# Kernel optimization log

Measured on AMD Instinct MI355X. Metric: run time of the kernel, lower is better.

Reference implementation:

```python
import jax, jax.numpy as jnp
import numpy as np

B, T, E, H, V = 64, 32, 300, 1024, 10000


def setup_inputs() -> dict:
    key = jax.random.key(0)
    ks = jax.random.split(key, 12)
    s = lambda fan: 1.0 / np.sqrt(fan)
    return {
        "questions": jax.random.randint(ks[0], (B, T), 0, V, dtype=jnp.int64) if jax.config.jax_enable_x64 else jax.random.randint(ks[0], (B, T), 0, V, dtype=jnp.int32),
        "question_lengths": jax.random.randint(ks[1], (B,), 1, T + 1, dtype=jnp.int32),
        "embed_table": jax.random.normal(ks[2], (V, E), jnp.float32) * 0.02,
        "W_ih1": jax.random.normal(ks[3], (4 * H, E), jnp.float32) * s(H),
        "W_hh1": jax.random.normal(ks[4], (4 * H, H), jnp.float32) * s(H),
        "b_ih1": jax.random.normal(ks[5], (4 * H,), jnp.float32) * s(H),
        "b_hh1": jax.random.normal(ks[6], (4 * H,), jnp.float32) * s(H),
        "W_ih2": jax.random.normal(ks[7], (4 * H, H), jnp.float32) * s(H),
        "W_hh2": jax.random.normal(ks[8], (4 * H, H), jnp.float32) * s(H),
        "b_ih2": jax.random.normal(ks[9], (4 * H,), jnp.float32) * s(H),
        "b_hh2": jax.random.normal(ks[10], (4 * H,), jnp.float32) * s(H),
    }


def _lstm_cell(x_t, h, c, W_ih, W_hh, b_ih, b_hh):
    # PyTorch LSTMCell: gate order i, f, g, o
    gates = x_t @ W_ih.T + b_ih + h @ W_hh.T + b_hh  # [B, 4H]
    i, f, g, o = jnp.split(gates, 4, axis=-1)
    c_new = jax.nn.sigmoid(f) * c + jax.nn.sigmoid(i) * jnp.tanh(g)
    h_new = jax.nn.sigmoid(o) * jnp.tanh(c_new)
    return h_new, c_new


def reference(questions, question_lengths, embed_table,
              W_ih1, W_hh1, b_ih1, b_hh1, W_ih2, W_hh2, b_ih2, b_hh2):
    x = embed_table[questions]                      # [B, T, E]
    b, t, _ = x.shape
    h = W_hh1.shape[1]

    def step(carry, inp):
        h1, c1, h2, c2 = carry
        x_t, m = inp                                # x_t [B,E], m [B,1] bool
        h1n, c1n = _lstm_cell(x_t, h1, c1, W_ih1, W_hh1, b_ih1, b_hh1)
        h2n, c2n = _lstm_cell(h1n, h2, c2, W_ih2, W_hh2, b_ih2, b_hh2)
        # samples past their length keep their final state frozen
        h1 = jnp.where(m, h1n, h1); c1 = jnp.where(m, c1n, c1)
        h2 = jnp.where(m, h2n, h2); c2 = jnp.where(m, c2n, c2)
        return (h1, c1, h2, c2), None

    mask = jnp.arange(t)[None, :] < question_lengths[:, None]      # [B,T]
    xs = (jnp.swapaxes(x, 0, 1), jnp.swapaxes(mask, 0, 1)[..., None])
    init = tuple(jnp.zeros((b, h), x.dtype) for _ in range(4))
    (h1, c1, h2, c2), _ = jax.lax.scan(step, init, xs)

    # tile final top-layer hidden to [B, H, 28, 28]
    E_q = jnp.broadcast_to(h2[:, None, None, :], (b, 28, 28, h))
    E_q = jnp.transpose(E_q, (0, 3, 2, 1))
    return (E_q, h1[:, None, :], h2[:, None, :], c1[:, None, :], c2[:, None, :])
```

## Files before the change

kernel.cpp:

```cpp
#include <hip/hip_runtime.h>
#include <hip/hip_bf16.h>
#include <cstdint>

#define B_  64
#define T_  32
#define E_  300
#define EP  320
#define H_  1024
#define G4  4096
#define BH  65536
#define NBLK 192

typedef __attribute__((ext_vector_type(8))) short bf16x8;
typedef __attribute__((ext_vector_type(4))) float f32x4;
typedef unsigned short ushort_t;

__device__ __forceinline__ bf16x8 load_b8(const ushort_t* p) {
    union { uint4 u; bf16x8 v; } c;
    c.u = *reinterpret_cast<const uint4*>(p);
    return c.v;
}

__device__ __forceinline__ ushort_t f2bf(float x) {
    union { float f; uint32_t u; } c; c.f = x;
    uint32_t r = c.u + 0x7fffu + ((c.u >> 16) & 1u);
    return (ushort_t)(r >> 16);
}

__device__ __forceinline__ float sigm(float x) { return 1.0f / (1.0f + __expf(-x)); }

__device__ __forceinline__ void astore64(uint64_t* p, uint64_t v) {
    __hip_atomic_store(p, v, __ATOMIC_RELAXED, __HIP_MEMORY_SCOPE_AGENT);
}
__device__ __forceinline__ uint64_t packf2(float a, float b) {
    union { float f[2]; uint64_t u; } c; c.f[0] = a; c.f[1] = b; return c.u;
}

__device__ __forceinline__ void setflag(int* flags, int role, int js, int val) {
    __hip_atomic_store(&flags[(role * 64 + js) * 16], val,
                       __ATOMIC_RELAXED, __HIP_MEMORY_SCOPE_AGENT);
}
__device__ __forceinline__ void waitwave(const int* flags, int role, int target, int lane) {
    const int* p = &flags[(role * 64 + lane) * 16];
    int guard = 0;
    for (;;) {
        int v = __hip_atomic_load(p, __ATOMIC_RELAXED, __HIP_MEMORY_SCOPE_AGENT);
        if (__all(v >= target)) return;
        if (++guard > (1 << 22)) return;
        __builtin_amdgcn_s_sleep(1);
    }
}

__global__ void prep_inputs(const int* __restrict__ q, const float* __restrict__ table,
                            ushort_t* __restrict__ Xp,
                            const float* __restrict__ Wsrc, ushort_t* __restrict__ Wdst,
                            ushort_t* __restrict__ h1s0, ushort_t* __restrict__ h2s0) {
    int blk = blockIdx.x;
    if (blk < 1280) {
        int i = blk * 256 + threadIdx.x;
        const int n = B_ * T_ * EP;
        for (; i < n; i += 1280 * 256) {
            int r = i / EP, c = i - r * EP;
            Xp[i] = (c < E_) ? f2bf(table[q[r] * E_ + c]) : (ushort_t)0;
        }
    } else if (blk < 3328) {
        int i = (blk - 1280) * 256 + threadIdx.x;
        const int n = G4 * EP;
        for (; i < n; i += 2048 * 256) {
            int r = i / EP, c = i - r * EP;
            Wdst[i] = (c < E_) ? f2bf(Wsrc[r * E_ + c]) : (ushort_t)0;
        }
    } else {
        int i = (blk - 3328) * 256 + threadIdx.x;
        uint4 z = make_uint4(0, 0, 0, 0);
        if (i < 8192) reinterpret_cast<uint4*>(h1s0)[i] = z;
        else          reinterpret_cast<uint4*>(h2s0)[i - 8192] = z;
    }
}

__launch_bounds__(256)
__global__ void xgemm(const ushort_t* __restrict__ Xp, const ushort_t* __restrict__ Wp,
                      const float* __restrict__ b_ih1, const float* __restrict__ b_hh1,
                      float* __restrict__ xg) {
    int mblk = blockIdx.x, nblk = blockIdx.y;
    int wave = threadIdx.x >> 6, lane = threadIdx.x & 63;
    int lm = lane & 15, lq = lane >> 4;
    int m0 = mblk * 64 + wave * 16;
    f32x4 acc[4];
    #pragma unroll
    for (int g = 0; g < 4; ++g) {
        int n = nblk * 64 + g * 16 + lm;
        float bv = b_ih1[n] + b_hh1[n];
        acc[g] = (f32x4){bv, bv, bv, bv};
    }
    for (int k0 = 0; k0 < EP; k0 += 32) {
        bf16x8 a = load_b8(Xp + (m0 + lm) * EP + k0 + lq * 8);
        #pragma unroll
        for (int g = 0; g < 4; ++g) {
            bf16x8 b = load_b8(Wp + (nblk * 64 + g * 16 + lm) * EP + k0 + lq * 8);
            acc[g] = __builtin_amdgcn_mfma_f32_16x16x32_bf16(a, b, acc[g], 0, 0, 0);
        }
    }
    #pragma unroll
    for (int g = 0; g < 4; ++g)
        #pragma unroll
        for (int r = 0; r < 4; ++r) {
            int m = m0 + lq * 4 + r;
            int b = m >> 5, t = m & 31;
            int n = nblk * 64 + g * 16 + lm;
            int gate = n >> 10, j = n & 1023;
            xg[(((size_t)t * B_ + b) * H_ + j) * 4 + gate] = acc[g][r];
        }
}


__device__ __forceinline__ void gemm_half(const ushort_t* __restrict__ hslot,
                                          const ushort_t* __restrict__ wsf,
                                          int lm, int lq, int m0, int kh, f32x4 acc[4]) {
    const uint4* hr = reinterpret_cast<const uint4*>(hslot);
    const int rbase = (m0 + lm) * 2 + (lq & 1);
    const int cbo = lq >> 1;
    const int cb0 = kh * 32;
    uint4 buf[16];
    #pragma unroll
    for (int grp = 0; grp < 2; ++grp)
        #pragma unroll
        for (int i = 0; i < 8; ++i)
            buf[grp * 8 + i] = hr[(cb0 + grp * 16 + i * 2 + cbo) * 128 + rbase];
    #pragma unroll
    for (int grp = 0; grp < 2; ++grp)
        #pragma unroll
        for (int i = 0; i < 8; ++i) {
            int k0 = kh * 512 + grp * 256 + i * 32;
            union { uint4 u; bf16x8 v; } a; a.u = buf[grp * 8 + i];
            #pragma unroll
            for (int g = 0; g < 4; ++g) {
                int row = g * 16 + lm;
                bf16x8 bb = load_b8(wsf + row * 1024 + ((k0 + lq * 8) ^ ((lm & 7) << 3)));
                acc[g] = __builtin_amdgcn_mfma_f32_16x16x32_bf16(a.v, bb, acc[g], 0, 0, 0);
            }
        }
}

__device__ __forceinline__ void lstm_elem(const f32x4 acc[4], int r,
                                          float* c, float* h, ushort_t* hb) {
    float iv = sigm(acc[0][r]);
    float fv = sigm(acc[1][r]);
    float gv = tanhf(acc[2][r]);
    float ov = sigm(acc[3][r]);
    float cn = fv * c[r] + iv * gv;
    float hv = ov * tanhf(cn);
    c[r] = cn; h[r] = hv; hb[r] = f2bf(hv);
}

__device__ __forceinline__ void store_h_tile(ushort_t* slot, int js, const ushort_t* hst) {
    int tid = threadIdx.x;
    uint64_t v = reinterpret_cast<const uint64_t*>(hst)[tid];
    astore64(reinterpret_cast<uint64_t*>(slot) + js * 256 + tid, v);
}

__global__ __launch_bounds__(512) void lstm_persist(
    const float* __restrict__ Whh1, const float* __restrict__ Wih2,
    const float* __restrict__ Whh2,
    const float* __restrict__ b_ih2, const float* __restrict__ b_hh2,
    const float* __restrict__ xg, const int* __restrict__ qlen,
    ushort_t* __restrict__ h1hist,
    ushort_t* __restrict__ h2hist,
    float* __restrict__ Qhist,
    float* __restrict__ h1f, float* __restrict__ c1f,
    float* __restrict__ h2f, float* __restrict__ c2f,
    int* __restrict__ flags)
{
    __shared__ ushort_t ws[64 * 1024];
    __shared__ __align__(16) ushort_t hstage[64][16];
    __shared__ f32x4 pacc[256][4];

    const int blk  = blockIdx.x;
    const int role = blk >> 6;
    const int js   = blk & 63;
    const int w    = threadIdx.x >> 6, lane = threadIdx.x & 63;
    const int mi   = w & 3, kh = w >> 2;
    const int lm = lane & 15, lq = lane >> 4;
    const int m0 = mi * 16;
    const int pidx = mi * 64 + lane;

    const float* Wsrc = (role == 0) ? Whh1 : (role == 1) ? Wih2 : Whh2;
    uint2* wsp = reinterpret_cast<uint2*>(ws);
    for (int idx = threadIdx.x; idx < 64 * 256; idx += 512) {
        int r = idx >> 8, c4 = idx & 255;
        int grow = (r >> 4) * H_ + js * 16 + (r & 15);
        float4 v = reinterpret_cast<const float4*>(Wsrc + (size_t)grow * H_)[c4];
        uint2 pk;
        pk.x = (uint32_t)f2bf(v.x) | ((uint32_t)f2bf(v.y) << 16);
        pk.y = (uint32_t)f2bf(v.z) | ((uint32_t)f2bf(v.w) << 16);
        wsp[r * 256 + (c4 ^ ((r & 7) << 1))] = pk;
    }
    __syncthreads();

    int q[4];
    #pragma unroll
    for (int r = 0; r < 4; ++r) q[r] = qlen[m0 + lq * 4 + r];

    float    c_reg[4]  = {0.f, 0.f, 0.f, 0.f};
    float    h_reg[4]  = {0.f, 0.f, 0.f, 0.f};
    ushort_t hb_reg[4] = {0, 0, 0, 0};

    if (role == 0) {
        for (int t = 0; t < T_; ++t) {
            f32x4 acc[4];
            #pragma unroll
            for (int g = 0; g < 4; ++g) acc[g] = (f32x4){0.f, 0.f, 0.f, 0.f};
            if (kh == 0) {
                uint4 xq[4];
                #pragma unroll
                for (int r = 0; r < 4; ++r)
                    xq[r] = reinterpret_cast<const uint4*>(xg)
                            [((size_t)t * B_ + (m0 + lq * 4 + r)) * H_ + js * 16 + lm];
                #pragma unroll
                for (int r = 0; r < 4; ++r) {
                    union { uint32_t u; float f; } x0, x1, x2, x3;
                    x0.u = xq[r].x; x1.u = xq[r].y; x2.u = xq[r].z; x3.u = xq[r].w;
                    acc[0][r] = x0.f; acc[1][r] = x1.f;
                    acc[2][r] = x2.f; acc[3][r] = x3.f;
                }
            }
            if (t > 0) {
                if (w == 0) waitwave(flags, 0, t, lane);
                __syncthreads();
            }
            gemm_half(h1hist + (size_t)t * BH, ws, lm, lq, m0, kh, acc);
            if (kh == 1) {
                #pragma unroll
                for (int g = 0; g < 4; ++g) pacc[pidx][g] = acc[g];
            }
            __syncthreads();
            if (kh == 0) {
                #pragma unroll
                for (int g = 0; g < 4; ++g) acc[g] += pacc[pidx][g];
                #pragma unroll
                for (int r = 0; r < 4; ++r) {
                    if (t < q[r]) lstm_elem(acc, r, c_reg, h_reg, hb_reg);
                    hstage[m0 + lq * 4 + r][lm] = hb_reg[r];
                }
            }
            __syncthreads();
            if (threadIdx.x < 256)
                store_h_tile(h1hist + (size_t)(t + 1) * BH, js, &hstage[0][0]);
            __syncthreads();
            if (threadIdx.x == 0) setflag(flags, 0, js, t + 1);
        }
        if (kh == 0) {
            #pragma unroll
            for (int r = 0; r < 4; ++r) {
                int b = m0 + lq * 4 + r, j = js * 16 + lm;
                h1f[b * H_ + j] = h_reg[r]; c1f[b * H_ + j] = c_reg[r];
            }
        }
    } else if (role == 1) {
        float bi[4];
        #pragma unroll
        for (int g = 0; g < 4; ++g) {
            int n = g * H_ + js * 16 + lm;
            bi[g] = b_ih2[n] + b_hh2[n];
        }
        for (int t = 0; t < T_; ++t) {
            if (w == 0) waitwave(flags, 0, t + 1, lane);
            __syncthreads();
            f32x4 acc[4];
            #pragma unroll
            for (int g = 0; g < 4; ++g)
                acc[g] = (kh == 0) ? (f32x4){bi[g], bi[g], bi[g], bi[g]}
                                   : (f32x4){0.f, 0.f, 0.f, 0.f};
            gemm_half(h1hist + (size_t)(t + 1) * BH, ws, lm, lq, m0, kh, acc);
            if (kh == 1) {
                #pragma unroll
                for (int g = 0; g < 4; ++g) pacc[pidx][g] = acc[g];
            }
            __syncthreads();
            if (kh == 0) {
                #pragma unroll
                for (int g = 0; g < 4; ++g) acc[g] += pacc[pidx][g];
                uint64_t* Qw64 = (uint64_t*)(Qhist + (size_t)t * (4 * BH));
                #pragma unroll
                for (int r = 0; r < 4; ++r) {
                    int b = m0 + lq * 4 + r, j = js * 16 + lm;
                    size_t base = ((size_t)b * H_ + j) * 2;
                    astore64(Qw64 + base,     packf2(acc[0][r], acc[1][r]));
                    astore64(Qw64 + base + 1, packf2(acc[2][r], acc[3][r]));
                }
            }
            __syncthreads();
            if (threadIdx.x == 0) setflag(flags, 1, js, t + 1);
        }
    } else {
        for (int t = 0; t < T_; ++t) {
            if (w == 0)               waitwave(flags, 1, t + 1, lane);
            else if (w == 1 && t > 0) waitwave(flags, 2, t,     lane);
            __syncthreads();
            uint4 qp[4];
            if (kh == 0) {
                const uint4* Qr = (const uint4*)(Qhist + (size_t)t * (4 * BH));
                #pragma unroll
                for (int r = 0; r < 4; ++r)
                    qp[r] = Qr[(size_t)(m0 + lq * 4 + r) * H_ + js * 16 + lm];
            }
            f32x4 acc[4];
            #pragma unroll
            for (int g = 0; g < 4; ++g) acc[g] = (f32x4){0.f, 0.f, 0.f, 0.f};
            gemm_half(h2hist + (size_t)t * BH, ws, lm, lq, m0, kh, acc);
            if (kh == 1) {
                #pragma unroll
                for (int g = 0; g < 4; ++g) pacc[pidx][g] = acc[g];
            }
            __syncthreads();
            if (kh == 0) {
                #pragma unroll
                for (int g = 0; g < 4; ++g) acc[g] += pacc[pidx][g];
                #pragma unroll
                for (int r = 0; r < 4; ++r) {
                    union { uint32_t u; float f; } x0, x1, x2, x3;
                    x0.u = qp[r].x; x1.u = qp[r].y; x2.u = qp[r].z; x3.u = qp[r].w;
                    acc[0][r] += x0.f; acc[1][r] += x1.f;
                    acc[2][r] += x2.f; acc[3][r] += x3.f;
                }
                #pragma unroll
                for (int r = 0; r < 4; ++r) {
                    if (t < q[r]) lstm_elem(acc, r, c_reg, h_reg, hb_reg);
                    hstage[m0 + lq * 4 + r][lm] = hb_reg[r];
                }
            }
            __syncthreads();
            if (threadIdx.x < 256)
                store_h_tile(h2hist + (size_t)(t + 1) * BH, js, &hstage[0][0]);
            __syncthreads();
            if (t < T_ - 1 && threadIdx.x == 0) setflag(flags, 2, js, t + 1);
        }
        if (kh == 0) {
            #pragma unroll
            for (int r = 0; r < 4; ++r) {
                int b = m0 + lq * 4 + r, j = js * 16 + lm;
                h2f[b * H_ + j] = h_reg[r]; c2f[b * H_ + j] = c_reg[r];
            }
        }
    }
}

__global__ void write_out(const float* __restrict__ h1f, const float* __restrict__ h2f,
                          const float* __restrict__ c1f, const float* __restrict__ c2f,
                          float* __restrict__ out) {
    const long long EQ = (long long)B_ * H_ * 784;
    const long long n4 = (EQ + 4LL * B_ * H_) / 4;
    long long i4 = (long long)blockIdx.x * blockDim.x + threadIdx.x;
    long long stride = (long long)gridDim.x * blockDim.x;
    for (; i4 < n4; i4 += stride) {
        long long f = i4 * 4;
        float4 v;
        if (f < EQ) {
            long long bh = f / 784;
            float val = h2f[bh];
            v = make_float4(val, val, val, val);
        } else {
            long long r = f - EQ;
            int which = (int)(r >> 16);
            int j = (int)(r & 65535);
            const float* src = (which == 0) ? h1f : (which == 1) ? h2f : (which == 2) ? c1f : c2f;
            v = *reinterpret_cast<const float4*>(src + j);
        }
        reinterpret_cast<float4*>(out)[i4] = v;
    }
}

extern "C" void kernel_launch(void* const* d_in, const int* in_sizes, int n_in,
                              void* d_out, int out_size, void* d_ws, size_t ws_size,
                              hipStream_t stream) {
    const int*   questions = (const int*)d_in[0];
    const int*   qlen      = (const int*)d_in[1];
    const float* embed     = (const float*)d_in[2];
    const float* W_ih1     = (const float*)d_in[3];
    const float* W_hh1     = (const float*)d_in[4];
    const float* b_ih1     = (const float*)d_in[5];
    const float* b_hh1     = (const float*)d_in[6];
    const float* W_ih2     = (const float*)d_in[7];
    const float* W_hh2     = (const float*)d_in[8];
    const float* b_ih2     = (const float*)d_in[9];
    const float* b_hh2     = (const float*)d_in[10];
    float* out = (float*)d_out;

    char* w = (char*)d_ws;
    float*    xg     = (float*)(w + 0);
    ushort_t* Wih1p  = (ushort_t*)(w + 33554432);
    ushort_t* Xp     = (ushort_t*)(w + 36175872);
    int*      flags  = (int*)(w + 36175872);
    ushort_t* h1hist = (ushort_t*)(w + 37486592);
    ushort_t* h2hist = (ushort_t*)(w + 41811968);
    float*    Qhist  = (float*)(w + 46137344);
    float*    h1f    = (float*)(w + 79691776);
    float*    c1f    = (float*)(w + 79953920);
    float*    h2f    = (float*)(w + 80216064);
    float*    c2f    = (float*)(w + 80478208);

    prep_inputs<<<3392, 256, 0, stream>>>(questions, embed, Xp, W_ih1, Wih1p,
                                          h1hist, h2hist);
    xgemm<<<dim3(32, 64), 256, 0, stream>>>(Xp, Wih1p, b_ih1, b_hh1, xg);

    hipMemsetAsync(w + 36175872, 0, 12288, stream);

    lstm_persist<<<NBLK, 512, 0, stream>>>(W_hh1, W_ih2, W_hh2, b_ih2, b_hh2,
                                           xg, qlen,
                                           h1hist, h2hist, Qhist,
                                           h1f, c1f, h2f, c2f, flags);

    write_out<<<4096, 256, 0, stream>>>(h1f, h2f, c1f, c2f, out);
}
```

Measured before the change: 529.3 us.

## Keep recurrent weight slices in registers and split K across four waves

The persistent LSTM kernel no longer stages its 64x1024 bf16 weight slice in shared memory. Each wave now holds its K-quarter of the weights as MFMA B-fragments in registers and covers two 16-row M tiles, so it no longer reads weights from LDS on every step. Partial sums from the four K-quarters are reduced through a smaller shared buffer, and the flag zeroing moves from a separate memset into the prep kernel at a new workspace offset. The cost is heavy register pressure (32 bf16x8 fragments plus accumulators per lane), which may cause spills, and a three-way LDS reduction on every step.

New measurement: 727.0 us. 1.37x slower.

```diff
diff --git a/kernel.cpp b/kernel.cpp
--- a/kernel.cpp
+++ b/kernel.cpp
@@ -54,7 +54,8 @@
 __global__ void prep_inputs(const int* __restrict__ q, const float* __restrict__ table,
                             ushort_t* __restrict__ Xp,
                             const float* __restrict__ Wsrc, ushort_t* __restrict__ Wdst,
-                            ushort_t* __restrict__ h1s0, ushort_t* __restrict__ h2s0) {
+                            ushort_t* __restrict__ h1s0, ushort_t* __restrict__ h2s0,
+                            int* __restrict__ flags) {
     int blk = blockIdx.x;
     if (blk < 1280) {
         int i = blk * 256 + threadIdx.x;
@@ -70,11 +71,14 @@
             int r = i / EP, c = i - r * EP;
             Wdst[i] = (c < E_) ? f2bf(Wsrc[r * E_ + c]) : (ushort_t)0;
         }
-    } else {
+    } else if (blk < 3392) {
         int i = (blk - 3328) * 256 + threadIdx.x;
         uint4 z = make_uint4(0, 0, 0, 0);
         if (i < 8192) reinterpret_cast<uint4*>(h1s0)[i] = z;
         else          reinterpret_cast<uint4*>(h2s0)[i - 8192] = z;
+    } else {
+        int i = (blk - 3392) * 256 + threadIdx.x;
+        reinterpret_cast<uint4*>(flags)[i] = make_uint4(0, 0, 0, 0);
     }
 }
 
@@ -114,43 +118,30 @@
 }
 
 
-__device__ __forceinline__ void gemm_half(const ushort_t* __restrict__ hslot,
-                                          const ushort_t* __restrict__ wsf,
-                                          int lm, int lq, int m0, int kh, f32x4 acc[4]) {
-    const uint4* hr = reinterpret_cast<const uint4*>(hslot);
-    const int rbase = (m0 + lm) * 2 + (lq & 1);
-    const int cbo = lq >> 1;
-    const int cb0 = kh * 32;
-    uint4 buf[16];
+__device__ __forceinline__ void gemm_q(const uint4* __restrict__ hr,
+                                       const bf16x8 (&wfr)[32],
+                                       int rbase, int cbase, f32x4 acc[2][4]) {
     #pragma unroll
-    for (int grp = 0; grp < 2; ++grp)
-        #pragma unroll
-        for (int i = 0; i < 8; ++i)
-            buf[grp * 8 + i] = hr[(cb0 + grp * 16 + i * 2 + cbo) * 128 + rbase];
-    #pragma unroll
-    for (int grp = 0; grp < 2; ++grp)
+    for (int half = 0; half < 2; ++half) {
+        uint4 af[8];
         #pragma unroll
         for (int i = 0; i < 8; ++i) {
-            int k0 = kh * 512 + grp * 256 + i * 32;
-            union { uint4 u; bf16x8 v; } a; a.u = buf[grp * 8 + i];
+            int kc = half * 4 + (i >> 1), mi = i & 1;
+            af[i] = hr[cbase + kc * 256 + rbase + mi * 32];
+        }
+        #pragma unroll
+        for (int k4 = 0; k4 < 4; ++k4) {
+            int kc = half * 4 + k4;
             #pragma unroll
-            for (int g = 0; g < 4; ++g) {
-                int row = g * 16 + lm;
-                bf16x8 bb = load_b8(wsf + row * 1024 + ((k0 + lq * 8) ^ ((lm & 7) << 3)));
-                acc[g] = __builtin_amdgcn_mfma_f32_16x16x32_bf16(a.v, bb, acc[g], 0, 0, 0);
-            }
-        }
-}
-
-__device__ __forceinline__ void lstm_elem(const f32x4 acc[4], int r,
-                                          float* c, float* h, ushort_t* hb) {
-    float iv = sigm(acc[0][r]);
-    float fv = sigm(acc[1][r]);
-    float gv = tanhf(acc[2][r]);
-    float ov = sigm(acc[3][r]);
-    float cn = fv * c[r] + iv * gv;
-    float hv = ov * tanhf(cn);
-    c[r] = cn; h[r] = hv; hb[r] = f2bf(hv);
+            for (int mi = 0; mi < 2; ++mi) {
+                union { uint4 u; bf16x8 v; } a; a.u = af[k4 * 2 + mi];
+                #pragma unroll
+                for (int nt = 0; nt < 4; ++nt)
+                    acc[mi][nt] = __builtin_amdgcn_mfma_f32_16x16x32_bf16(
+                        a.v, wfr[nt * 8 + kc], acc[mi][nt], 0, 0, 0);
+            }
+        }
+    }
 }
 
 __device__ __forceinline__ void store_h_tile(ushort_t* slot, int js, const ushort_t* hst) {
@@ -159,7 +150,7 @@
     astore64(reinterpret_cast<uint64_t*>(slot) + js * 256 + tid, v);
 }
 
-__global__ __launch_bounds__(512) void lstm_persist(
+__global__ __launch_bounds__(512, 2) void lstm_persist(
     const float* __restrict__ Whh1, const float* __restrict__ Wih2,
     const float* __restrict__ Whh2,
     const float* __restrict__ b_ih2, const float* __restrict__ b_hh2,
@@ -171,77 +162,103 @@
     float* __restrict__ h2f, float* __restrict__ c2f,
     int* __restrict__ flags)
 {
-    __shared__ ushort_t ws[64 * 1024];
+    __shared__ f32x4 pacc[8][6][64];
     __shared__ __align__(16) ushort_t hstage[64][16];
-    __shared__ f32x4 pacc[256][4];
 
     const int blk  = blockIdx.x;
     const int role = blk >> 6;
     const int js   = blk & 63;
     const int w    = threadIdx.x >> 6, lane = threadIdx.x & 63;
-    const int mi   = w & 3, kh = w >> 2;
+    const int kq   = w & 3, mh = w >> 2;
     const int lm = lane & 15, lq = lane >> 4;
-    const int m0 = mi * 16;
-    const int pidx = mi * 64 + lane;
 
     const float* Wsrc = (role == 0) ? Whh1 : (role == 1) ? Wih2 : Whh2;
-    uint2* wsp = reinterpret_cast<uint2*>(ws);
-    for (int idx = threadIdx.x; idx < 64 * 256; idx += 512) {
-        int r = idx >> 8, c4 = idx & 255;
-        int grow = (r >> 4) * H_ + js * 16 + (r & 15);
-        float4 v = reinterpret_cast<const float4*>(Wsrc + (size_t)grow * H_)[c4];
-        uint2 pk;
-        pk.x = (uint32_t)f2bf(v.x) | ((uint32_t)f2bf(v.y) << 16);
-        pk.y = (uint32_t)f2bf(v.z) | ((uint32_t)f2bf(v.w) << 16);
-        wsp[r * 256 + (c4 ^ ((r & 7) << 1))] = pk;
-    }
-    __syncthreads();
-
-    int q[4];
+    bf16x8 wfr[32];
     #pragma unroll
-    for (int r = 0; r < 4; ++r) q[r] = qlen[m0 + lq * 4 + r];
-
-    float    c_reg[4]  = {0.f, 0.f, 0.f, 0.f};
-    float    h_reg[4]  = {0.f, 0.f, 0.f, 0.f};
-    ushort_t hb_reg[4] = {0, 0, 0, 0};
+    for (int nt = 0; nt < 4; ++nt)
+        #pragma unroll
+        for (int kc = 0; kc < 8; ++kc) {
+            const float* p = Wsrc + (size_t)(nt * H_ + js * 16 + lm) * H_
+                           + kq * 256 + kc * 32 + lq * 8;
+            float4 v0 = *reinterpret_cast<const float4*>(p);
+            float4 v1 = *reinterpret_cast<const float4*>(p + 4);
+            union { uint32_t u[4]; bf16x8 v; } c;
+            c.u[0] = (uint32_t)f2bf(v0.x) | ((uint32_t)f2bf(v0.y) << 16);
+            c.u[1] = (uint32_t)f2bf(v0.z) | ((uint32_t)f2bf(v0.w) << 16);
+            c.u[2] = (uint32_t)f2bf(v1.x) | ((uint32_t)f2bf(v1.y) << 16);
+            c.u[3] = (uint32_t)f2bf(v1.z) | ((uint32_t)f2bf(v1.w) << 16);
+            wfr[nt * 8 + kc] = c.v;
+        }
+
+    const int rbase = (mh * 32 + lm) * 2 + (lq & 1);
+    const int cbase = (kq * 16 + (lq >> 1)) * 128;
+
+    int q[2][4];
+    #pragma unroll
+    for (int mi = 0; mi < 2; ++mi)
+        #pragma unroll
+        for (int r = 0; r < 4; ++r)
+            q[mi][r] = qlen[mh * 32 + mi * 16 + lq * 4 + r];
+
+    float    c_reg[2][4] = {};
+    float    h_reg[2][4] = {};
+    ushort_t hb_reg[2][4] = {};
 
     if (role == 0) {
         for (int t = 0; t < T_; ++t) {
-            f32x4 acc[4];
-            #pragma unroll
-            for (int g = 0; g < 4; ++g) acc[g] = (f32x4){0.f, 0.f, 0.f, 0.f};
-            if (kh == 0) {
-                uint4 xq[4];
-                #pragma unroll
-                for (int r = 0; r < 4; ++r)
-                    xq[r] = reinterpret_cast<const uint4*>(xg)
-                            [((size_t)t * B_ + (m0 + lq * 4 + r)) * H_ + js * 16 + lm];
-                #pragma unroll
-                for (int r = 0; r < 4; ++r) {
-                    union { uint32_t u; float f; } x0, x1, x2, x3;
-                    x0.u = xq[r].x; x1.u = xq[r].y; x2.u = xq[r].z; x3.u = xq[r].w;
-                    acc[0][r] = x0.f; acc[1][r] = x1.f;
-                    acc[2][r] = x2.f; acc[3][r] = x3.f;
-                }
-            }
             if (t > 0) {
                 if (w == 0) waitwave(flags, 0, t, lane);
                 __syncthreads();
             }
-            gemm_half(h1hist + (size_t)t * BH, ws, lm, lq, m0, kh, acc);
-            if (kh == 1) {
-                #pragma unroll
-                for (int g = 0; g < 4; ++g) pacc[pidx][g] = acc[g];
-            }
-            __syncthreads();
-            if (kh == 0) {
-                #pragma unroll
-                for (int g = 0; g < 4; ++g) acc[g] += pacc[pidx][g];
-                #pragma unroll
-                for (int r = 0; r < 4; ++r) {
-                    if (t < q[r]) lstm_elem(acc, r, c_reg, h_reg, hb_reg);
-                    hstage[m0 + lq * 4 + r][lm] = hb_reg[r];
-                }
+            f32x4 acc[2][4] = {};
+            gemm_q(reinterpret_cast<const uint4*>(h1hist + (size_t)t * BH),
+                   wfr, rbase, cbase, acc);
+            uint4 xq[8];
+            if (kq == 0) {
+                #pragma unroll
+                for (int mi = 0; mi < 2; ++mi)
+                    #pragma unroll
+                    for (int r = 0; r < 4; ++r)
+                        xq[mi * 4 + r] = reinterpret_cast<const uint4*>(xg)
+                            [((size_t)t * B_ + (mh * 32 + mi * 16 + lq * 4 + r)) * H_ + js * 16 + lm];
+            } else {
+                #pragma unroll
+                for (int mi = 0; mi < 2; ++mi)
+                    #pragma unroll
+                    for (int nt = 0; nt < 4; ++nt)
+                        pacc[mi * 4 + nt][mh * 3 + (kq - 1)][lane] = acc[mi][nt];
+            }
+            __syncthreads();
+            if (kq == 0) {
+                #pragma unroll
+                for (int s = 0; s < 3; ++s)
+                    #pragma unroll
+                    for (int mi = 0; mi < 2; ++mi)
+                        #pragma unroll
+                        for (int nt = 0; nt < 4; ++nt)
+                            acc[mi][nt] += pacc[mi * 4 + nt][mh * 3 + s][lane];
+                #pragma unroll
+                for (int mi = 0; mi < 2; ++mi)
+                    #pragma unroll
+                    for (int r = 0; r < 4; ++r) {
+                        union { uint32_t u; float f; } x0, x1, x2, x3;
+                        x0.u = xq[mi * 4 + r].x; x1.u = xq[mi * 4 + r].y;
+                        x2.u = xq[mi * 4 + r].z; x3.u = xq[mi * 4 + r].w;
+                        float a0 = acc[0][0][0];
+                        (void)a0;
+                        float g0 = acc[mi][0][r] + x0.f;
+                        float g1 = acc[mi][1][r] + x1.f;
+                        float g2 = acc[mi][2][r] + x2.f;
+                        float g3 = acc[mi][3][r] + x3.f;
+                        if (t < q[mi][r]) {
+                            float iv = sigm(g0), fv = sigm(g1);
+                            float gv = tanhf(g2), ov = sigm(g3);
+                            float cn = fv * c_reg[mi][r] + iv * gv;
+                            float hv = ov * tanhf(cn);
+                            c_reg[mi][r] = cn; h_reg[mi][r] = hv; hb_reg[mi][r] = f2bf(hv);
+                        }
+                        hstage[mh * 32 + mi * 16 + lq * 4 + r][lm] = hb_reg[mi][r];
+                    }
             }
             __syncthreads();
             if (threadIdx.x < 256)
@@ -249,12 +266,14 @@
             __syncthreads();
             if (threadIdx.x == 0) setflag(flags, 0, js, t + 1);
         }
-        if (kh == 0) {
+        if (kq == 0) {
             #pragma unroll
-            for (int r = 0; r < 4; ++r) {
-                int b = m0 + lq * 4 + r, j = js * 16 + lm;
-                h1f[b * H_ + j] = h_reg[r]; c1f[b * H_ + j] = c_reg[r];
-            }
+            for (int mi = 0; mi < 2; ++mi)
+                #pragma unroll
+                for (int r = 0; r < 4; ++r) {
+                    int b = mh * 32 + mi * 16 + lq * 4 + r, j = js * 16 + lm;
+                    h1f[b * H_ + j] = h_reg[mi][r]; c1f[b * H_ + j] = c_reg[mi][r];
+                }
         }
     } else if (role == 1) {
         float bi[4];
@@ -266,28 +285,37 @@
         for (int t = 0; t < T_; ++t) {
             if (w == 0) waitwave(flags, 0, t + 1, lane);
             __syncthreads();
-            f32x4 acc[4];
-            #pragma unroll
-            for (int g = 0; g < 4; ++g)
-                acc[g] = (kh == 0) ? (f32x4){bi[g], bi[g], bi[g], bi[g]}
-                                   : (f32x4){0.f, 0.f, 0.f, 0.f};
-            gemm_half(h1hist + (size_t)(t + 1) * BH, ws, lm, lq, m0, kh, acc);
-            if (kh == 1) {
-                #pragma unroll
-                for (int g = 0; g < 4; ++g) pacc[pidx][g] = acc[g];
-            }
-            __syncthreads();
-            if (kh == 0) {
-                #pragma unroll
-                for (int g = 0; g < 4; ++g) acc[g] += pacc[pidx][g];
+            f32x4 acc[2][4] = {};
+            gemm_q(reinterpret_cast<const uint4*>(h1hist + (size_t)(t + 1) * BH),
+                   wfr, rbase, cbase, acc);
+            if (kq != 0) {
+                #pragma unroll
+                for (int mi = 0; mi < 2; ++mi)
+                    #pragma unroll
+                    for (int nt = 0; nt < 4; ++nt)
+                        pacc[mi * 4 + nt][mh * 3 + (kq - 1)][lane] = acc[mi][nt];
+            }
+            __syncthreads();
+            if (kq == 0) {
+                #pragma unroll
+                for (int s = 0; s < 3; ++s)
+                    #pragma unroll
+                    for (int mi = 0; mi < 2; ++mi)
+                        #pragma unroll
+                        for (int nt = 0; nt < 4; ++nt)
+                            acc[mi][nt] += pacc[mi * 4 + nt][mh * 3 + s][lane];
                 uint64_t* Qw64 = (uint64_t*)(Qhist + (size_t)t * (4 * BH));
                 #pragma unroll
-                for (int r = 0; r < 4; ++r) {
-                    int b = m0 + lq * 4 + r, j = js * 16 + lm;
-                    size_t base = ((size_t)b * H_ + j) * 2;
-                    astore64(Qw64 + base,     packf2(acc[0][r], acc[1][r]));
-                    astore64(Qw64 + base + 1, packf2(acc[2][r], acc[3][r]));
-                }
+                for (int mi = 0; mi < 2; ++mi)
+                    #pragma unroll
+                    for (int r = 0; r < 4; ++r) {
+                        int b = mh * 32 + mi * 16 + lq * 4 + r, j = js * 16 + lm;
+                        size_t base = ((size_t)b * H_ + j) * 2;
+                        astore64(Qw64 + base,
+                                 packf2(acc[mi][0][r] + bi[0], acc[mi][1][r] + bi[1]));
+                        astore64(Qw64 + base + 1,
+                                 packf2(acc[mi][2][r] + bi[2], acc[mi][3][r] + bi[3]));
+                    }
             }
             __syncthreads();
             if (threadIdx.x == 0) setflag(flags, 1, js, t + 1);
@@ -297,37 +325,53 @@
             if (w == 0)               waitwave(flags, 1, t + 1, lane);
             else if (w == 1 && t > 0) waitwave(flags, 2, t,     lane);
             __syncthreads();
-            uint4 qp[4];
-            if (kh == 0) {
+            f32x4 acc[2][4] = {};
+            gemm_q(reinterpret_cast<const uint4*>(h2hist + (size_t)t * BH),
+                   wfr, rbase, cbase, acc);
+            uint4 qp[8];
+            if (kq == 0) {
                 const uint4* Qr = (const uint4*)(Qhist + (size_t)t * (4 * BH));
                 #pragma unroll
-                for (int r = 0; r < 4; ++r)
-                    qp[r] = Qr[(size_t)(m0 + lq * 4 + r) * H_ + js * 16 + lm];
-            }
-            f32x4 acc[4];
-            #pragma unroll
-            for (int g = 0; g < 4; ++g) acc[g] = (f32x4){0.f, 0.f, 0.f, 0.f};
-            gemm_half(h2hist + (size_t)t * BH, ws, lm, lq, m0, kh, acc);
-            if (kh == 1) {
-                #pragma unroll
-                for (int g = 0; g < 4; ++g) pacc[pidx][g] = acc[g];
-            }
-            __syncthreads();
-            if (kh == 0) {
-                #pragma unroll
-                for (int g = 0; g < 4; ++g) acc[g] += pacc[pidx][g];
-                #pragma unroll
-                for (int r = 0; r < 4; ++r) {
-                    union { uint32_t u; float f; } x0, x1, x2, x3;
-                    x0.u = qp[r].x; x1.u = qp[r].y; x2.u = qp[r].z; x3.u = qp[r].w;
-                    acc[0][r] += x0.f; acc[1][r] += x1.f;
-                    acc[2][r] += x2.f; acc[3][r] += x3.f;
-                }
-                #pragma unroll
-                for (int r = 0; r < 4; ++r) {
-                    if (t < q[r]) lstm_elem(acc, r, c_reg, h_reg, hb_reg);
-                    hstage[m0 + lq * 4 + r][lm] = hb_reg[r];
-                }
+                for (int mi = 0; mi < 2; ++mi)
+                    #pragma unroll
+                    for (int r = 0; r < 4; ++r)
+                        qp[mi * 4 + r] = Qr[(size_t)(mh * 32 + mi * 16 + lq * 4 + r) * H_ + js * 16 + lm];
+            } else {
+                #pragma unroll
+                for (int mi = 0; mi < 2; ++mi)
+                    #pragma unroll
+                    for (int nt = 0; nt < 4; ++nt)
+                        pacc[mi * 4 + nt][mh * 3 + (kq - 1)][lane] = acc[mi][nt];
+            }
+            __syncthreads();
+            if (kq == 0) {
+                #pragma unroll
+                for (int s = 0; s < 3; ++s)
+                    #pragma unroll
+                    for (int mi = 0; mi < 2; ++mi)
+                        #pragma unroll
+                        for (int nt = 0; nt < 4; ++nt)
+                            acc[mi][nt] += pacc[mi * 4 + nt][mh * 3 + s][lane];
+                #pragma unroll
+                for (int mi = 0; mi < 2; ++mi)
+                    #pragma unroll
+                    for (int r = 0; r < 4; ++r) {
+                        union { uint32_t u; float f; } x0, x1, x2, x3;
+                        x0.u = qp[mi * 4 + r].x; x1.u = qp[mi * 4 + r].y;
+                        x2.u = qp[mi * 4 + r].z; x3.u = qp[mi * 4 + r].w;
+                        float g0 = acc[mi][0][r] + x0.f;
+                        float g1 = acc[mi][1][r] + x1.f;
+                        float g2 = acc[mi][2][r] + x2.f;
+                        float g3 = acc[mi][3][r] + x3.f;
+                        if (t < q[mi][r]) {
+                            float iv = sigm(g0), fv = sigm(g1);
+                            float gv = tanhf(g2), ov = sigm(g3);
+                            float cn = fv * c_reg[mi][r] + iv * gv;
+                            float hv = ov * tanhf(cn);
+                            c_reg[mi][r] = cn; h_reg[mi][r] = hv; hb_reg[mi][r] = f2bf(hv);
+                        }
+                        hstage[mh * 32 + mi * 16 + lq * 4 + r][lm] = hb_reg[mi][r];
+                    }
             }
             __syncthreads();
             if (threadIdx.x < 256)
@@ -335,12 +379,14 @@
             __syncthreads();
             if (t < T_ - 1 && threadIdx.x == 0) setflag(flags, 2, js, t + 1);
         }
-        if (kh == 0) {
+        if (kq == 0) {
             #pragma unroll
-            for (int r = 0; r < 4; ++r) {
-                int b = m0 + lq * 4 + r, j = js * 16 + lm;
-                h2f[b * H_ + j] = h_reg[r]; c2f[b * H_ + j] = c_reg[r];
-            }
+            for (int mi = 0; mi < 2; ++mi)
+                #pragma unroll
+                for (int r = 0; r < 4; ++r) {
+                    int b = mh * 32 + mi * 16 + lq * 4 + r, j = js * 16 + lm;
+                    h2f[b * H_ + j] = h_reg[mi][r]; c2f[b * H_ + j] = c_reg[mi][r];
+                }
         }
     }
 }
@@ -390,7 +436,6 @@
     float*    xg     = (float*)(w + 0);
     ushort_t* Wih1p  = (ushort_t*)(w + 33554432);
     ushort_t* Xp     = (ushort_t*)(w + 36175872);
-    int*      flags  = (int*)(w + 36175872);
     ushort_t* h1hist = (ushort_t*)(w + 37486592);
     ushort_t* h2hist = (ushort_t*)(w + 41811968);
     float*    Qhist  = (float*)(w + 46137344);
@@ -398,12 +443,11 @@
     float*    c1f    = (float*)(w + 79953920);
     float*    h2f    = (float*)(w + 80216064);
     float*    c2f    = (float*)(w + 80478208);
-
-    prep_inputs<<<3392, 256, 0, stream>>>(questions, embed, Xp, W_ih1, Wih1p,
-                                          h1hist, h2hist);
+    int*      flags  = (int*)(w + 80740352);
+
+    prep_inputs<<<3395, 256, 0, stream>>>(questions, embed, Xp, W_ih1, Wih1p,
+                                          h1hist, h2hist, flags);
     xgemm<<<dim3(32, 64), 256, 0, stream>>>(Xp, Wih1p, b_ih1, b_hh1, xg);
-
-    hipMemsetAsync(w + 36175872, 0, 12288, stream);
 
     lstm_persist<<<NBLK, 512, 0, stream>>>(W_hh1, W_ih2, W_hh2, b_ih2, b_hh2,
                                            xg, qlen,
```

## Fuse output writes into persistent LSTM kernel and fold flag reset into prep

Applied to the files above, without the earlier changes.

Drops the separate write_out kernel. Each sample's final h/c states and its broadcast 28x28 E_q tile are now written from inside the persistent LSTM kernel, at the timestep where that sample's length ends. The flag memset moves into extra blocks of prep_inputs, removing two launches. The cost is that the roughly 205 MB E_q broadcast now runs inside the latency-bound recurrence loop on only 64 blocks, which could stretch the critical path.

Result: slower. 607.8 us (+14.8%).

```diff
diff --git a/kernel.cpp b/kernel.cpp
--- a/kernel.cpp
+++ b/kernel.cpp
@@ -11,6 +11,12 @@
 #define BH  65536
 #define NBLK 192
 
+#define EQOFF 0LL
+#define H1OFF 51380224LL
+#define H2OFF 51445760LL
+#define C1OFF 51511296LL
+#define C2OFF 51576832LL
+
 typedef __attribute__((ext_vector_type(8))) short bf16x8;
 typedef __attribute__((ext_vector_type(4))) float f32x4;
 typedef unsigned short ushort_t;
@@ -54,7 +60,8 @@
 __global__ void prep_inputs(const int* __restrict__ q, const float* __restrict__ table,
                             ushort_t* __restrict__ Xp,
                             const float* __restrict__ Wsrc, ushort_t* __restrict__ Wdst,
-                            ushort_t* __restrict__ h1s0, ushort_t* __restrict__ h2s0) {
+                            ushort_t* __restrict__ h1s0, ushort_t* __restrict__ h2s0,
+                            int* __restrict__ flags) {
     int blk = blockIdx.x;
     if (blk < 1280) {
         int i = blk * 256 + threadIdx.x;
@@ -70,11 +77,14 @@
             int r = i / EP, c = i - r * EP;
             Wdst[i] = (c < E_) ? f2bf(Wsrc[r * E_ + c]) : (ushort_t)0;
         }
-    } else {
+    } else if (blk < 3392) {
         int i = (blk - 3328) * 256 + threadIdx.x;
         uint4 z = make_uint4(0, 0, 0, 0);
         if (i < 8192) reinterpret_cast<uint4*>(h1s0)[i] = z;
         else          reinterpret_cast<uint4*>(h2s0)[i - 8192] = z;
+    } else {
+        int i = (blk - 3392) * 256 + threadIdx.x;
+        reinterpret_cast<uint4*>(flags)[i] = make_uint4(0, 0, 0, 0);
     }
 }
 
@@ -167,13 +177,14 @@
     ushort_t* __restrict__ h1hist,
     ushort_t* __restrict__ h2hist,
     float* __restrict__ Qhist,
-    float* __restrict__ h1f, float* __restrict__ c1f,
-    float* __restrict__ h2f, float* __restrict__ c2f,
+    float* __restrict__ out,
     int* __restrict__ flags)
 {
     __shared__ ushort_t ws[64 * 1024];
     __shared__ __align__(16) ushort_t hstage[64][16];
     __shared__ f32x4 pacc[256][4];
+    __shared__ float hstage32[64][16];
+    __shared__ int qlen_sh[64];
 
     const int blk  = blockIdx.x;
     const int role = blk >> 6;
@@ -183,6 +194,8 @@
     const int lm = lane & 15, lq = lane >> 4;
     const int m0 = mi * 16;
     const int pidx = mi * 64 + lane;
+
+    if (threadIdx.x < 64) qlen_sh[threadIdx.x] = qlen[threadIdx.x];
 
     const float* Wsrc = (role == 0) ? Whh1 : (role == 1) ? Wih2 : Whh2;
     uint2* wsp = reinterpret_cast<uint2*>(ws);
@@ -199,7 +212,7 @@
 
     int q[4];
     #pragma unroll
-    for (int r = 0; r < 4; ++r) q[r] = qlen[m0 + lq * 4 + r];
+    for (int r = 0; r < 4; ++r) q[r] = qlen_sh[m0 + lq * 4 + r];
 
     float    c_reg[4]  = {0.f, 0.f, 0.f, 0.f};
     float    h_reg[4]  = {0.f, 0.f, 0.f, 0.f};
@@ -248,12 +261,15 @@
                 store_h_tile(h1hist + (size_t)(t + 1) * BH, js, &hstage[0][0]);
             __syncthreads();
             if (threadIdx.x == 0) setflag(flags, 0, js, t + 1);
-        }
-        if (kh == 0) {
-            #pragma unroll
-            for (int r = 0; r < 4; ++r) {
-                int b = m0 + lq * 4 + r, j = js * 16 + lm;
-                h1f[b * H_ + j] = h_reg[r]; c1f[b * H_ + j] = c_reg[r];
+            if (kh == 0) {
+                #pragma unroll
+                for (int r = 0; r < 4; ++r) {
+                    if (q[r] == t + 1) {
+                        int b = m0 + lq * 4 + r, j = js * 16 + lm;
+                        out[H1OFF + b * H_ + j] = h_reg[r];
+                        out[C1OFF + b * H_ + j] = c_reg[r];
+                    }
+                }
             }
         }
     } else if (role == 1) {
@@ -327,6 +343,7 @@
                 for (int r = 0; r < 4; ++r) {
                     if (t < q[r]) lstm_elem(acc, r, c_reg, h_reg, hb_reg);
                     hstage[m0 + lq * 4 + r][lm] = hb_reg[r];
+                    hstage32[m0 + lq * 4 + r][lm] = h_reg[r];
                 }
             }
             __syncthreads();
@@ -334,39 +351,27 @@
                 store_h_tile(h2hist + (size_t)(t + 1) * BH, js, &hstage[0][0]);
             __syncthreads();
             if (t < T_ - 1 && threadIdx.x == 0) setflag(flags, 2, js, t + 1);
-        }
-        if (kh == 0) {
-            #pragma unroll
-            for (int r = 0; r < 4; ++r) {
-                int b = m0 + lq * 4 + r, j = js * 16 + lm;
-                h2f[b * H_ + j] = h_reg[r]; c2f[b * H_ + j] = c_reg[r];
-            }
-        }
-    }
-}
-
-__global__ void write_out(const float* __restrict__ h1f, const float* __restrict__ h2f,
-                          const float* __restrict__ c1f, const float* __restrict__ c2f,
-                          float* __restrict__ out) {
-    const long long EQ = (long long)B_ * H_ * 784;
-    const long long n4 = (EQ + 4LL * B_ * H_) / 4;
-    long long i4 = (long long)blockIdx.x * blockDim.x + threadIdx.x;
-    long long stride = (long long)gridDim.x * blockDim.x;
-    for (; i4 < n4; i4 += stride) {
-        long long f = i4 * 4;
-        float4 v;
-        if (f < EQ) {
-            long long bh = f / 784;
-            float val = h2f[bh];
-            v = make_float4(val, val, val, val);
-        } else {
-            long long r = f - EQ;
-            int which = (int)(r >> 16);
-            int j = (int)(r & 65535);
-            const float* src = (which == 0) ? h1f : (which == 1) ? h2f : (which == 2) ? c1f : c2f;
-            v = *reinterpret_cast<const float4*>(src + j);
-        }
-        reinterpret_cast<float4*>(out)[i4] = v;
+            if (kh == 0) {
+                #pragma unroll
+                for (int r = 0; r < 4; ++r) {
+                    if (q[r] == t + 1) {
+                        int b = m0 + lq * 4 + r, j = js * 16 + lm;
+                        out[H2OFF + b * H_ + j] = h_reg[r];
+                        out[C2OFF + b * H_ + j] = c_reg[r];
+                    }
+                }
+            }
+            for (int b = 0; b < B_; ++b) {
+                if (qlen_sh[b] != t + 1) continue;
+                float4* dst = reinterpret_cast<float4*>(
+                    out + (size_t)b * (H_ * 784) + (size_t)js * 16 * 784);
+                for (int idx = threadIdx.x; idx < 3136; idx += 512) {
+                    int c = idx / 196, p4 = idx - c * 196;
+                    float v = hstage32[b][c];
+                    dst[c * 196 + p4] = make_float4(v, v, v, v);
+                }
+            }
+        }
     }
 }
 
@@ -390,25 +395,17 @@
     float*    xg     = (float*)(w + 0);
     ushort_t* Wih1p  = (ushort_t*)(w + 33554432);
     ushort_t* Xp     = (ushort_t*)(w + 36175872);
-    int*      flags  = (int*)(w + 36175872);
     ushort_t* h1hist = (ushort_t*)(w + 37486592);
     ushort_t* h2hist = (ushort_t*)(w + 41811968);
     float*    Qhist  = (float*)(w + 46137344);
-    float*    h1f    = (float*)(w + 79691776);
-    float*    c1f    = (float*)(w + 79953920);
-    float*    h2f    = (float*)(w + 80216064);
-    float*    c2f    = (float*)(w + 80478208);
-
-    prep_inputs<<<3392, 256, 0, stream>>>(questions, embed, Xp, W_ih1, Wih1p,
-                                          h1hist, h2hist);
+    int*      flags  = (int*)(w + 80740352);
+
+    prep_inputs<<<3395, 256, 0, stream>>>(questions, embed, Xp, W_ih1, Wih1p,
+                                          h1hist, h2hist, flags);
     xgemm<<<dim3(32, 64), 256, 0, stream>>>(Xp, Wih1p, b_ih1, b_hh1, xg);
-
-    hipMemsetAsync(w + 36175872, 0, 12288, stream);
 
     lstm_persist<<<NBLK, 512, 0, stream>>>(W_hh1, W_ih2, W_hh2, b_ih2, b_hh2,
                                            xg, qlen,
                                            h1hist, h2hist, Qhist,
-                                           h1f, c1f, h2f, c2f, flags);
-
-    write_out<<<4096, 256, 0, stream>>>(h1f, h2f, c1f, c2f, out);
-}
+                                           out, flags);
+}
```
